# Kernel optimization log

Measured on AMD Instinct MI355X. Metric: run time of the kernel, lower is better.

The kernel has to match this reference:

```python
import jax, jax.numpy as jnp
import numpy as np

MEM_LEN = 1024
EPS = 1e-5


def _layer_norm(x, g, b):
    mu = jnp.mean(x, axis=-1, keepdims=True)
    var = jnp.mean((x - mu) ** 2, axis=-1, keepdims=True)
    return (x - mu) * jax.lax.rsqrt(var + EPS) * g + b


def _rel_shift(t):
    # t: [B, H, T, L] -> TXL pad->view->slice->view shift
    B, H, T, L = t.shape
    padded = jnp.concatenate([jnp.zeros((B, H, T, 1), t.dtype), t], axis=-1)
    padded = padded.reshape(B, H, L + 1, T)
    return padded[:, :, 1:, :].reshape(B, H, T, L)


def _pos_emb(length, d_model, dtype):
    inv_freq = 1.0 / (10000.0 ** (np.arange(0, d_model, 2, dtype=np.float32) / d_model))
    pos_seq = np.arange(length - 1, -1, -1, dtype=np.float32)
    sin_inp = np.outer(pos_seq, inv_freq)
    pe = np.concatenate([np.sin(sin_inp), np.cos(sin_inp)], axis=-1)
    return jnp.asarray(pe, dtype=dtype)


def setup_inputs() -> dict:
    key = jax.random.key(0)
    ks = jax.random.split(key, 12)
    B, T, M, D, H, Dff = 4, 1024, 1024, 1024, 16, 4096
    dh = D // H
    s = 1.0 / np.sqrt(D)
    return {
        "x": jax.random.normal(ks[0], (B, T, D), jnp.float32),
        "mem": jax.random.normal(ks[1], (B, M, D), jnp.float32),
        "Wq": jax.random.normal(ks[2], (D, D), jnp.float32) * s,
        "Wk": jax.random.normal(ks[3], (D, D), jnp.float32) * s,
        "Wv": jax.random.normal(ks[4], (D, D), jnp.float32) * s,
        "Wr": jax.random.normal(ks[5], (D, D), jnp.float32) * s,
        "Wo": jax.random.normal(ks[6], (D, D), jnp.float32) * s,
        "bias_u": jax.random.normal(ks[7], (H, dh), jnp.float32) * 0.02,
        "bias_v": jax.random.normal(ks[8], (H, dh), jnp.float32) * 0.02,
        "ln1_g": jnp.ones((D,), jnp.float32),
        "ln1_b": jnp.zeros((D,), jnp.float32),
        "ln2_g": jnp.ones((D,), jnp.float32),
        "ln2_b": jnp.zeros((D,), jnp.float32),
        "W1": jax.random.normal(ks[9], (D, Dff), jnp.float32) * s,
        "b1": jnp.zeros((Dff,), jnp.float32),
        "W2": jax.random.normal(ks[10], (Dff, D), jnp.float32) * (1.0 / np.sqrt(Dff)),
        "b2": jnp.zeros((D,), jnp.float32),
    }


def reference(x, mem, Wq, Wk, Wv, Wr, Wo, bias_u, bias_v,
              ln1_g, ln1_b, ln2_g, ln2_b, W1, b1, W2, b2):
    B, T, D = x.shape
    M = mem.shape[1]
    H, dh = bias_u.shape
    L = T + M
    scale = 1.0 / np.sqrt(dh)

    residual = x
    xn = _layer_norm(x, ln1_g, ln1_b)

    cat = jnp.concatenate([mem_n := mem, xn], axis=1) if False else jnp.concatenate([mem, xn], axis=1)
    # NOTE: torch concatenates raw memory states (not re-normalized) with norm_x.
    k = (cat @ Wk).reshape(B, L, H, dh).transpose(0, 2, 1, 3)      # [B,H,L,dh]
    v = (cat @ Wv).reshape(B, L, H, dh).transpose(0, 2, 1, 3)      # [B,H,L,dh]
    q = (xn @ Wq).reshape(B, T, H, dh).transpose(0, 2, 1, 3)       # [B,H,T,dh]

    pe = _pos_emb(L, D, x.dtype)                                   # [L,D]
    r = (pe @ Wr).reshape(L, H, dh).transpose(1, 0, 2)             # [H,L,dh]

    content = jnp.einsum("bhid,bhjd->bhij", q + bias_u[None, :, None, :], k)
    rel = jnp.einsum("bhid,hjd->bhij", q + bias_v[None, :, None, :], r)
    rel = _rel_shift(rel)

    attn = jax.nn.softmax((content + rel) * scale, axis=-1)        # [B,H,T,L]
    out = jnp.einsum("bhij,bhjd->bhid", attn, v)                   # [B,H,T,dh]
    out = out.transpose(0, 2, 1, 3).reshape(B, T, D) @ Wo

    x2 = residual + out
    xf = _layer_norm(x2, ln2_g, ln2_b)
    ff = jax.nn.gelu(xf @ W1 + b1, approximate=False) @ W2 + b2
    y = x2 + ff

    new_mem = jax.lax.stop_gradient(
        jnp.concatenate([mem, residual], axis=1)[:, -MEM_LEN:])
    return y, new_mem
```

## Files before the change

kernel.cpp:

```cpp
#include <hip/hip_runtime.h>
#include <hip/hip_bf16.h>

typedef short bf16x8 __attribute__((ext_vector_type(8)));
typedef float f32x4 __attribute__((ext_vector_type(4)));
typedef unsigned short u16;

__device__ __forceinline__ float bf2f(u16 u) {
    union { unsigned int i; float f; } x; x.i = ((unsigned int)u) << 16; return x.f;
}
__device__ __forceinline__ u16 f2bf(float f) {
    union { float f; unsigned int i; } x; x.f = f;
    unsigned int r = x.i + 0x7fff + ((x.i >> 16) & 1);
    return (u16)(r >> 16);
}
__device__ __forceinline__ f32x4 mfma16(bf16x8 a, bf16x8 b, f32x4 c) {
    return __builtin_amdgcn_mfma_f32_16x16x32_bf16(a, b, c, 0, 0, 0);
}
#define GLL16(lds_base, gsrc) \
    __builtin_amdgcn_global_load_lds((const __attribute__((address_space(1))) void*)(gsrc), \
                                     (__attribute__((address_space(3))) void*)(lds_base), 16, 0, 0)

__global__ __launch_bounds__(256)
void transpose_kernel(const float* __restrict__ in, u16* __restrict__ out, int R, int C) {
    __shared__ float t[32][33];
    const int c0 = blockIdx.x * 32, r0 = blockIdx.y * 32;
    const int tx = threadIdx.x & 31, ty = threadIdx.x >> 5;
#pragma unroll
    for (int i = 0; i < 32; i += 8) t[ty + i][tx] = in[(size_t)(r0 + ty + i) * C + c0 + tx];
    __syncthreads();
#pragma unroll
    for (int i = 0; i < 32; i += 8) out[(size_t)(c0 + ty + i) * R + r0 + tx] = f2bf(t[tx][ty + i]);
}

__global__ __launch_bounds__(256)
void convert_kernel(const float* __restrict__ in, u16* __restrict__ out) {
    const size_t i = ((size_t)blockIdx.x * 256 + threadIdx.x) * 8;
    const float4 a = *(const float4*)(in + i);
    const float4 b = *(const float4*)(in + i + 4);
    bf16x8 o;
    o[0] = (short)f2bf(a.x); o[1] = (short)f2bf(a.y);
    o[2] = (short)f2bf(a.z); o[3] = (short)f2bf(a.w);
    o[4] = (short)f2bf(b.x); o[5] = (short)f2bf(b.y);
    o[6] = (short)f2bf(b.z); o[7] = (short)f2bf(b.w);
    *(bf16x8*)(out + i) = o;
}

__global__ __launch_bounds__(256)
void pe_kernel(u16* __restrict__ pe) {
    const int idx = blockIdx.x * 256 + threadIdx.x;
    const int p = idx >> 10, d = idx & 1023;
    const float pos = (float)(2047 - p);
    const int k = d & 511;
    const float invf = powf(10000.f, ((float)(2 * k)) * (-1.f / 1024.f));
    const float a = pos * invf;
    pe[idx] = f2bf((d < 512) ? sinf(a) : cosf(a));
}

__global__ __launch_bounds__(256)
void ln_kernel(const float* __restrict__ inp, const float* __restrict__ gg,
               const float* __restrict__ bb, u16* __restrict__ outp) {
    const int row = blockIdx.x * 4 + (threadIdx.x >> 6);
    const int l = threadIdx.x & 63;
    const size_t base = (size_t)row * 1024 + l * 16;
    float v[16];
    const float4* p4 = (const float4*)(inp + base);
#pragma unroll
    for (int j = 0; j < 4; ++j) {
        float4 f = p4[j];
        v[j*4+0] = f.x; v[j*4+1] = f.y; v[j*4+2] = f.z; v[j*4+3] = f.w;
    }
    float s = 0.f, s2 = 0.f;
#pragma unroll
    for (int j = 0; j < 16; ++j) { s += v[j]; s2 += v[j] * v[j]; }
#pragma unroll
    for (int off = 1; off < 64; off <<= 1) {
        s += __shfl_xor(s, off, 64);
        s2 += __shfl_xor(s2, off, 64);
    }
    const float mu = s * 0.0009765625f;
    const float var = s2 * 0.0009765625f - mu * mu;
    const float rs = rsqrtf(var + 1e-5f);
#pragma unroll
    for (int j = 0; j < 16; ++j)
        outp[base + j] = f2bf((v[j] - mu) * rs * gg[l * 16 + j] + bb[l * 16 + j]);
}

template<int EPI, bool CATA>
__global__ __launch_bounds__(256)
void gemm_kernel(const u16* __restrict__ A, const u16* __restrict__ A2,
                 const u16* __restrict__ Wt, void* __restrict__ outp,
                 u16* __restrict__ out2, const float* __restrict__ cb1,
                 const float* __restrict__ cb2, const float* __restrict__ residp,
                 int Mdim, int Ndim, int Kdim) {
    __shared__ __attribute__((aligned(16))) u16 As[128 * 32];
    __shared__ __attribute__((aligned(16))) u16 Bs[128 * 32];
    const int tid = threadIdx.x;
    const int w = tid >> 6, l = tid & 63;
    const int wr = w >> 1, wc = w & 1;
    const int m0 = blockIdx.x * 128, n0 = blockIdx.y * 128;
    f32x4 acc[4][4] = {};

    for (int k0 = 0; k0 < Kdim; k0 += 32) {
        __syncthreads();
#pragma unroll
        for (int p = 0; p < 2; ++p) {
            const int ebase = (p * 4 + w) * 512;
            const int e = ebase + l * 8;
            const int row = e >> 5, colk = e & 31;
            const u16* srcA;
            if (CATA) {
                const int rr = m0 + row;
                const int bb_ = rr >> 11, pos = rr & 2047;
                srcA = (pos < 1024 ? A + ((size_t)(bb_ * 1024 + pos)) * 1024
                                   : A2 + ((size_t)(bb_ * 1024 + pos - 1024)) * 1024)
                       + (k0 + colk);
            } else {
                srcA = A + (size_t)(m0 + row) * Kdim + (k0 + colk);
            }
            const u16* srcB = Wt + (size_t)(n0 + row) * Kdim + (k0 + colk);
            GLL16(&As[ebase], srcA);
            GLL16(&Bs[ebase], srcB);
        }
        __syncthreads();
        bf16x8 af[4], bfr[4];
#pragma unroll
        for (int mi = 0; mi < 4; ++mi)
            af[mi] = *(const bf16x8*)&As[(wr * 64 + mi * 16 + (l & 15)) * 32 + (l >> 4) * 8];
#pragma unroll
        for (int ni = 0; ni < 4; ++ni)
            bfr[ni] = *(const bf16x8*)&Bs[(wc * 64 + ni * 16 + (l & 15)) * 32 + (l >> 4) * 8];
#pragma unroll
        for (int mi = 0; mi < 4; ++mi)
#pragma unroll
            for (int ni = 0; ni < 4; ++ni)
                acc[mi][ni] = mfma16(af[mi], bfr[ni], acc[mi][ni]);
    }

#pragma unroll
    for (int mi = 0; mi < 4; ++mi)
#pragma unroll
        for (int ni = 0; ni < 4; ++ni)
#pragma unroll
            for (int rg = 0; rg < 4; ++rg) {
                const int row = m0 + wr * 64 + mi * 16 + (l >> 4) * 4 + rg;
                const int col = n0 + wc * 64 + ni * 16 + (l & 15);
                const size_t idx = (size_t)row * Ndim + col;
                const float v = acc[mi][ni][rg];
                if (EPI == 0) {
                    ((u16*)outp)[idx] = f2bf(v);
                } else if (EPI == 1) {
                    ((u16*)outp)[idx] = f2bf(v + cb1[col]);
                    out2[idx] = f2bf(v + cb2[col]);
                } else if (EPI == 2) {
                    ((float*)outp)[idx] = v + residp[idx];
                } else if (EPI == 3) {
                    const float t = v + cb1[col];
                    ((u16*)outp)[idx] = f2bf(0.5f * t * (1.f + erff(t * 0.70710678118654752f)));
                } else {
                    ((float*)outp)[idx] = v + cb1[col] + residp[idx];
                }
            }
}

__global__ __launch_bounds__(256, 2)
void attn_kernel(const u16* __restrict__ qu, const u16* __restrict__ qv,
                 const u16* __restrict__ kcat, const u16* __restrict__ vcat,
                 const u16* __restrict__ rbuf, u16* __restrict__ outp) {
    constexpr int T = 1024, L = 2048, MM = 1024;
    __shared__ __attribute__((aligned(16))) u16 KtL[64 * 64];
    __shared__ __attribute__((aligned(16))) u16 RmL[128 * 64];
    __shared__ __attribute__((aligned(16))) u16 RwL[128 * 64];
    __shared__ __attribute__((aligned(16))) u16 Vt[64][72];
    __shared__ __attribute__((aligned(16))) u16 Pl[4][16][72];
    const int bid = blockIdx.x;
    const int g = (bid & 7) + 8 * (bid >> 7);
    const int it = (bid >> 3) & 15;
    const int h = g & 15, b = g >> 4;
    const int i0 = it * 64;
    const int tid = threadIdx.x;
    const int w = tid >> 6, l = tid & 63;
    const int lg = l >> 4, ll = l & 15;
    const int iw0 = i0 + w * 16;
    const int l8 = l >> 3;
    const int ssrc = ((l & 7) * 8) ^ (l8 << 3);
    const int sA = (lg * 8) ^ ((ll & 7) << 3);
    const int sB = (lg * 8 + 32) ^ ((ll & 7) << 3);

    bf16x8 quf[2], qvf[2];
    const int qc = h * 64 + lg * 8;
    {
        const size_t qrow = (size_t)(b * T + iw0 + ll);
        quf[0] = *(const bf16x8*)&qu[qrow * 1024 + qc];
        quf[1] = *(const bf16x8*)&qu[qrow * 1024 + qc + 32];
        qvf[0] = *(const bf16x8*)&qv[qrow * 1024 + qc];
        qvf[1] = *(const bf16x8*)&qv[qrow * 1024 + qc + 32];
    }
    const int r2 = iw0 + ll + 1;
    const size_t qrow2 = (size_t)(b * T + (r2 < T ? r2 : T - 1));
    const u16* kb = kcat + (size_t)b * L * 1024 + h * 64;
    const u16* vb = vcat + (size_t)b * L * 1024 + h * 64;
    const u16* rb = rbuf + h * 64;

    f32x4 o_acc[4] = {};
    float m_run[4] = {-1e30f, -1e30f, -1e30f, -1e30f};
    float l_run[4] = {0.f, 0.f, 0.f, 0.f};
    const int vjq = tid & 15, vdg = tid >> 4;

    for (int jt = 0; jt < 32; ++jt) {
        const int j0 = jt * 64;
        const bool main_blk = (j0 <= MM + i0 + 63);
        const bool wrap_blk = (j0 + 63 >= MM + i0 + 2);
        __syncthreads();
#pragma unroll
        for (int p = 0; p < 2; ++p) {
            const int k8 = w * 2 + p;
            GLL16(&KtL[k8 * 512], kb + (size_t)(j0 + k8 * 8 + l8) * 1024 + ssrc);
        }
        if (main_blk) {
            const long bm = (long)j0 + T - i0 - 64;
#pragma unroll
            for (int p = 0; p < 4; ++p) {
                const int k8 = w * 4 + p;
                GLL16(&RmL[k8 * 512], rb + (long)(bm + k8 * 8 + l8) * 1024 + ssrc);
            }
        }
        if (wrap_blk) {
            const long bw_ = (long)j0 - MM - i0 - 65;
#pragma unroll
            for (int p = 0; p < 4; ++p) {
                const int k8 = w * 4 + p;
                GLL16(&RwL[k8 * 512], rb + (long)(bw_ + k8 * 8 + l8) * 1024 + ssrc);
            }
        }
        {
            const u16* srcv = vb + (size_t)(j0 + vjq * 4) * 1024 + vdg * 4;
            const ushort4 r0 = *(const ushort4*)(srcv);
            const ushort4 r1 = *(const ushort4*)(srcv + 1024);
            const ushort4 r2w = *(const ushort4*)(srcv + 2048);
            const ushort4 r3 = *(const ushort4*)(srcv + 3072);
            const ushort4 c0 = {r0.x, r1.x, r2w.x, r3.x};
            const ushort4 c1 = {r0.y, r1.y, r2w.y, r3.y};
            const ushort4 c2 = {r0.z, r1.z, r2w.z, r3.z};
            const ushort4 c3 = {r0.w, r1.w, r2w.w, r3.w};
            *(ushort4*)&Vt[vdg * 4 + 0][vjq * 4] = c0;
            *(ushort4*)&Vt[vdg * 4 + 1][vjq * 4] = c1;
            *(ushort4*)&Vt[vdg * 4 + 2][vjq * 4] = c2;
            *(ushort4*)&Vt[vdg * 4 + 3][vjq * 4] = c3;
        }
        __syncthreads();

        f32x4 sv[4];
        __builtin_amdgcn_s_setprio(1);
#pragma unroll
        for (int ns = 0; ns < 4; ++ns) {
            const int rowb = (ns * 16 + ll) * 64;
            f32x4 a = {0.f, 0.f, 0.f, 0.f};
            a = mfma16(quf[0], *(const bf16x8*)&KtL[rowb + sA], a);
            a = mfma16(quf[1], *(const bf16x8*)&KtL[rowb + sB], a);
            sv[ns] = a;
        }
        __builtin_amdgcn_s_setprio(0);

        if (j0 <= MM + iw0 + 15) {
            const int trb = 48 - 16 * w;
            f32x4 gb[5];
#pragma unroll
            for (int cs = 0; cs < 5; ++cs) {
                const int rowb = (trb + cs * 16 + ll) * 64;
                f32x4 a = {0.f, 0.f, 0.f, 0.f};
                a = mfma16(qvf[0], *(const bf16x8*)&RmL[rowb + sA], a);
                a = mfma16(qvf[1], *(const bf16x8*)&RmL[rowb + sB], a);
                gb[cs] = a;
            }
#pragma unroll
            for (int r = 0; r < 4; ++r) {
                const int i_loc = lg * 4 + r;
                const int ig = iw0 + i_loc;
#pragma unroll
                for (int ns = 0; ns < 4; ++ns) {
                    const int j_loc = ns * 16 + ll;
                    const int c = j_loc + 15 - i_loc;
                    const int srcl = (l & 48) | (c & 15);
                    const float t0 = __shfl(gb[ns][r], srcl, 64);
                    const float t1 = __shfl(gb[ns + 1][r], srcl, 64);
                    const float gm = ((c >> 4) == ns) ? t0 : t1;
                    if (j0 + j_loc <= MM + ig) sv[ns][r] += gm;
                }
            }
        }
        if (j0 + 63 >= MM + iw0 + 2) {
            const bf16x8 qv2f0 = *(const bf16x8*)&qv[qrow2 * 1024 + qc];
            const bf16x8 qv2f1 = *(const bf16x8*)&qv[qrow2 * 1024 + qc + 32];
            const int trb = 48 - 16 * w;
            f32x4 gb[5];
#pragma unroll
            for (int cs = 0; cs < 5; ++cs) {
                const int rowb = (trb + cs * 16 + ll) * 64;
                f32x4 a = {0.f, 0.f, 0.f, 0.f};
                a = mfma16(qv2f0, *(const bf16x8*)&RwL[rowb + sA], a);
                a = mfma16(qv2f1, *(const bf16x8*)&RwL[rowb + sB], a);
                gb[cs] = a;
            }
#pragma unroll
            for (int r = 0; r < 4; ++r) {
                const int i_loc = lg * 4 + r;
                const int ig = iw0 + i_loc;
#pragma unroll
                for (int ns = 0; ns < 4; ++ns) {
                    const int j_loc = ns * 16 + ll;
                    const int c = j_loc + 15 - i_loc;
                    const int srcl = (l & 48) | (c & 15);
                    const float t0 = __shfl(gb[ns][r], srcl, 64);
                    const float t1 = __shfl(gb[ns + 1][r], srcl, 64);
                    const float gw = ((c >> 4) == ns) ? t0 : t1;
                    if (j0 + j_loc >= MM + ig + 2) sv[ns][r] += gw;
                }
            }
        }

#pragma unroll
        for (int r = 0; r < 4; ++r) {
            const int i_loc = lg * 4 + r;
            float s0 = sv[0][r] * 0.125f, s1 = sv[1][r] * 0.125f;
            float s2 = sv[2][r] * 0.125f, s3 = sv[3][r] * 0.125f;
            float pm = fmaxf(fmaxf(s0, s1), fmaxf(s2, s3));
            pm = fmaxf(pm, __shfl_xor(pm, 1, 64));
            pm = fmaxf(pm, __shfl_xor(pm, 2, 64));
            pm = fmaxf(pm, __shfl_xor(pm, 4, 64));
            pm = fmaxf(pm, __shfl_xor(pm, 8, 64));
            const float mnew = fmaxf(m_run[r], pm);
            const float alpha = __expf(m_run[r] - mnew);
            const float p0 = __expf(s0 - mnew), p1 = __expf(s1 - mnew);
            const float p2 = __expf(s2 - mnew), p3 = __expf(s3 - mnew);
            Pl[w][i_loc][0 * 16 + ll] = f2bf(p0);
            Pl[w][i_loc][1 * 16 + ll] = f2bf(p1);
            Pl[w][i_loc][2 * 16 + ll] = f2bf(p2);
            Pl[w][i_loc][3 * 16 + ll] = f2bf(p3);
            float ps = p0 + p1 + p2 + p3;
            ps += __shfl_xor(ps, 1, 64);
            ps += __shfl_xor(ps, 2, 64);
            ps += __shfl_xor(ps, 4, 64);
            ps += __shfl_xor(ps, 8, 64);
            l_run[r] = l_run[r] * alpha + ps;
            m_run[r] = mnew;
#pragma unroll
            for (int ns = 0; ns < 4; ++ns) o_acc[ns][r] *= alpha;
        }

        __builtin_amdgcn_s_setprio(1);
        const bf16x8 ap0 = *(const bf16x8*)&Pl[w][ll][lg * 8];
        const bf16x8 ap1 = *(const bf16x8*)&Pl[w][ll][32 + lg * 8];
#pragma unroll
        for (int ns = 0; ns < 4; ++ns) {
            const bf16x8 bv0 = *(const bf16x8*)&Vt[ns * 16 + ll][lg * 8];
            const bf16x8 bv1 = *(const bf16x8*)&Vt[ns * 16 + ll][32 + lg * 8];
            o_acc[ns] = mfma16(ap0, bv0, o_acc[ns]);
            o_acc[ns] = mfma16(ap1, bv1, o_acc[ns]);
        }
        __builtin_amdgcn_s_setprio(0);
    }

#pragma unroll
    for (int ns = 0; ns < 4; ++ns)
#pragma unroll
        for (int r = 0; r < 4; ++r) {
            const int row = iw0 + lg * 4 + r;
            outp[(size_t)(b * T + row) * 1024 + h * 64 + ns * 16 + ll] =
                f2bf(o_acc[ns][r] / l_run[r]);
        }
}

extern "C" void kernel_launch(void* const* d_in, const int* in_sizes, int n_in,
                              void* d_out, int out_size, void* d_ws, size_t ws_size,
                              hipStream_t stream) {
    const float* x    = (const float*)d_in[0];
    const float* mem  = (const float*)d_in[1];
    const float* Wq   = (const float*)d_in[2];
    const float* Wk   = (const float*)d_in[3];
    const float* Wv   = (const float*)d_in[4];
    const float* Wr   = (const float*)d_in[5];
    const float* Wo   = (const float*)d_in[6];
    const float* bu   = (const float*)d_in[7];
    const float* bv   = (const float*)d_in[8];
    const float* ln1g = (const float*)d_in[9];
    const float* ln1b = (const float*)d_in[10];
    const float* ln2g = (const float*)d_in[11];
    const float* ln2b = (const float*)d_in[12];
    const float* W1   = (const float*)d_in[13];
    const float* b1   = (const float*)d_in[14];
    const float* W2   = (const float*)d_in[15];
    const float* b2   = (const float*)d_in[16];

    float* y_out   = (float*)d_out;
    float* mem_out = (float*)d_out + 4194304;

    char* dob = (char*)d_out;
    u16* attno     = (u16*)(dob + 0);
    u16* pe        = (u16*)(dob + (size_t)8  * 1048576);
    u16* rbuf_base = (u16*)(dob + (size_t)12 * 1048576);
    u16* rbuf      = rbuf_base + 80 * 1024;
    char* dw = dob + (size_t)16 * 1048576 + 524288;
    u16* WqT = (u16*)(dw);
    u16* WkT = (u16*)(dw + (size_t)2 * 1048576);
    u16* WvT = (u16*)(dw + (size_t)4 * 1048576);
    u16* WrT = (u16*)(dw + (size_t)6 * 1048576);
    u16* WoT = (u16*)(dw + (size_t)8 * 1048576);

    char* ws = (char*)d_ws;
    const size_t MB = 1u << 20;
    u16*  xn    = (u16*)(ws + 0 * MB);
    u16*  x2n   = (u16*)(ws + 0 * MB);
    u16*  W2T   = (u16*)(ws + 0 * MB);
    u16*  qu    = (u16*)(ws + 8 * MB);
    float* x2f  = (float*)(ws + 8 * MB);
    u16*  qv    = (u16*)(ws + 16 * MB);
    u16*  kcat  = (u16*)(ws + 24 * MB);
    u16*  ffh   = (u16*)(ws + 24 * MB);
    u16*  vcat  = (u16*)(ws + 40 * MB);
    u16*  memb  = (u16*)(ws + 56 * MB);
    u16*  W1T   = (u16*)(ws + 56 * MB);

    transpose_kernel<<<dim3(32, 32), 256, 0, stream>>>(Wq, WqT, 1024, 1024);
    transpose_kernel<<<dim3(32, 32), 256, 0, stream>>>(Wk, WkT, 1024, 1024);
    transpose_kernel<<<dim3(32, 32), 256, 0, stream>>>(Wv, WvT, 1024, 1024);
    transpose_kernel<<<dim3(32, 32), 256, 0, stream>>>(Wr, WrT, 1024, 1024);
    transpose_kernel<<<dim3(32, 32), 256, 0, stream>>>(Wo, WoT, 1024, 1024);
    pe_kernel<<<8192, 256, 0, stream>>>(pe);
    convert_kernel<<<2048, 256, 0, stream>>>(mem, memb);
    ln_kernel<<<1024, 256, 0, stream>>>(x, ln1g, ln1b, xn);
    gemm_kernel<0, false><<<dim3(16, 8), 256, 0, stream>>>(pe, nullptr, WrT, rbuf, nullptr, nullptr, nullptr, nullptr, 2048, 1024, 1024);
    gemm_kernel<1, false><<<dim3(32, 8), 256, 0, stream>>>(xn, nullptr, WqT, qu, qv, bu, bv, nullptr, 4096, 1024, 1024);
    gemm_kernel<0, true><<<dim3(64, 8), 256, 0, stream>>>(memb, xn, WkT, kcat, nullptr, nullptr, nullptr, nullptr, 8192, 1024, 1024);
    gemm_kernel<0, true><<<dim3(64, 8), 256, 0, stream>>>(memb, xn, WvT, vcat, nullptr, nullptr, nullptr, nullptr, 8192, 1024, 1024);
    attn_kernel<<<1024, 256, 0, stream>>>(qu, qv, kcat, vcat, rbuf, attno);
    gemm_kernel<2, false><<<dim3(32, 8), 256, 0, stream>>>(attno, nullptr, WoT, x2f, nullptr, nullptr, nullptr, x, 4096, 1024, 1024);
    transpose_kernel<<<dim3(128, 32), 256, 0, stream>>>(W1, W1T, 1024, 4096);
    hipMemcpyAsync(mem_out, x, (size_t)4194304 * 4, hipMemcpyDeviceToDevice, stream);
    ln_kernel<<<1024, 256, 0, stream>>>(x2f, ln2g, ln2b, x2n);
    gemm_kernel<3, false><<<dim3(32, 32), 256, 0, stream>>>(x2n, nullptr, W1T, ffh, nullptr, b1, nullptr, nullptr, 4096, 4096, 1024);
    transpose_kernel<<<dim3(32, 128), 256, 0, stream>>>(W2, W2T, 4096, 1024);
    gemm_kernel<4, false><<<dim3(32, 8), 256, 0, stream>>>(ffh, nullptr, W2T, y_out, nullptr, b2, nullptr, x2f, 4096, 1024, 4096);
    (void)in_sizes; (void)n_in; (void)out_size; (void)ws_size;
}
```

Baseline: 599.8 us.

## Process 128 query rows per attention block so K/V/R tiles are reused twice

Each attention workgroup now covers 128 query rows instead of 64, with every wave handling two 16-row groups, so each K, V and positional tile loaded into LDS feeds twice as many rows. The grid is halved to 512 blocks and the launch bound drops to one block per SIMD-set, allowing more registers. The relative-position gather is also restructured to shuffle five sources once per row and select per column, instead of shuffling twice per column. In exchange, the larger LDS and register footprint lowers occupancy and gives fewer blocks to spread across the CUs. The rbuf padding offset is adjusted to match the larger R window.

```diff
diff --git a/kernel.cpp b/kernel.cpp
--- a/kernel.cpp
+++ b/kernel.cpp
@@ -162,53 +162,54 @@
             }
 }
 
-__global__ __launch_bounds__(256, 2)
+__global__ __launch_bounds__(256, 1)
 void attn_kernel(const u16* __restrict__ qu, const u16* __restrict__ qv,
                  const u16* __restrict__ kcat, const u16* __restrict__ vcat,
                  const u16* __restrict__ rbuf, u16* __restrict__ outp) {
     constexpr int T = 1024, L = 2048, MM = 1024;
     __shared__ __attribute__((aligned(16))) u16 KtL[64 * 64];
-    __shared__ __attribute__((aligned(16))) u16 RmL[128 * 64];
-    __shared__ __attribute__((aligned(16))) u16 RwL[128 * 64];
+    __shared__ __attribute__((aligned(16))) u16 RmL[192 * 64];
+    __shared__ __attribute__((aligned(16))) u16 RwL[192 * 64];
     __shared__ __attribute__((aligned(16))) u16 Vt[64][72];
-    __shared__ __attribute__((aligned(16))) u16 Pl[4][16][72];
+    __shared__ __attribute__((aligned(16))) u16 Pl[4][32][72];
     const int bid = blockIdx.x;
-    const int g = (bid & 7) + 8 * (bid >> 7);
-    const int it = (bid >> 3) & 15;
+    const int it = bid >> 6;
+    const int g = bid & 63;
     const int h = g & 15, b = g >> 4;
-    const int i0 = it * 64;
+    const int i0 = it * 128;
     const int tid = threadIdx.x;
     const int w = tid >> 6, l = tid & 63;
     const int lg = l >> 4, ll = l & 15;
-    const int iw0 = i0 + w * 16;
     const int l8 = l >> 3;
     const int ssrc = ((l & 7) * 8) ^ (l8 << 3);
     const int sA = (lg * 8) ^ ((ll & 7) << 3);
     const int sB = (lg * 8 + 32) ^ ((ll & 7) << 3);
-
-    bf16x8 quf[2], qvf[2];
     const int qc = h * 64 + lg * 8;
-    {
-        const size_t qrow = (size_t)(b * T + iw0 + ll);
-        quf[0] = *(const bf16x8*)&qu[qrow * 1024 + qc];
-        quf[1] = *(const bf16x8*)&qu[qrow * 1024 + qc + 32];
-        qvf[0] = *(const bf16x8*)&qv[qrow * 1024 + qc];
-        qvf[1] = *(const bf16x8*)&qv[qrow * 1024 + qc + 32];
+
+    bf16x8 quf[2][2], qvf[2][2];
+#pragma unroll
+    for (int rg = 0; rg < 2; ++rg) {
+        const size_t qrow = (size_t)(b * T + i0 + (w * 2 + rg) * 16 + ll);
+        quf[rg][0] = *(const bf16x8*)&qu[qrow * 1024 + qc];
+        quf[rg][1] = *(const bf16x8*)&qu[qrow * 1024 + qc + 32];
+        qvf[rg][0] = *(const bf16x8*)&qv[qrow * 1024 + qc];
+        qvf[rg][1] = *(const bf16x8*)&qv[qrow * 1024 + qc + 32];
     }
-    const int r2 = iw0 + ll + 1;
-    const size_t qrow2 = (size_t)(b * T + (r2 < T ? r2 : T - 1));
     const u16* kb = kcat + (size_t)b * L * 1024 + h * 64;
     const u16* vb = vcat + (size_t)b * L * 1024 + h * 64;
     const u16* rb = rbuf + h * 64;
 
-    f32x4 o_acc[4] = {};
-    float m_run[4] = {-1e30f, -1e30f, -1e30f, -1e30f};
-    float l_run[4] = {0.f, 0.f, 0.f, 0.f};
+    f32x4 o_acc[2][4] = {};
+    float m_run[2][4], l_run[2][4];
+#pragma unroll
+    for (int rg = 0; rg < 2; ++rg)
+#pragma unroll
+        for (int r = 0; r < 4; ++r) { m_run[rg][r] = -1e30f; l_run[rg][r] = 0.f; }
     const int vjq = tid & 15, vdg = tid >> 4;
 
     for (int jt = 0; jt < 32; ++jt) {
         const int j0 = jt * 64;
-        const bool main_blk = (j0 <= MM + i0 + 63);
+        const bool main_blk = (j0 <= MM + i0 + 127);
         const bool wrap_blk = (j0 + 63 >= MM + i0 + 2);
         __syncthreads();
 #pragma unroll
@@ -217,18 +218,18 @@
             GLL16(&KtL[k8 * 512], kb + (size_t)(j0 + k8 * 8 + l8) * 1024 + ssrc);
         }
         if (main_blk) {
-            const long bm = (long)j0 + T - i0 - 64;
-#pragma unroll
-            for (int p = 0; p < 4; ++p) {
-                const int k8 = w * 4 + p;
+            const long bm = (long)j0 + T - i0 - 128;
+#pragma unroll
+            for (int p = 0; p < 6; ++p) {
+                const int k8 = w * 6 + p;
                 GLL16(&RmL[k8 * 512], rb + (long)(bm + k8 * 8 + l8) * 1024 + ssrc);
             }
         }
         if (wrap_blk) {
-            const long bw_ = (long)j0 - MM - i0 - 65;
-#pragma unroll
-            for (int p = 0; p < 4; ++p) {
-                const int k8 = w * 4 + p;
+            const long bw_ = (long)j0 - MM - i0 - 129;
+#pragma unroll
+            for (int p = 0; p < 6; ++p) {
+                const int k8 = w * 6 + p;
                 GLL16(&RwL[k8 * 512], rb + (long)(bw_ + k8 * 8 + l8) * 1024 + ssrc);
             }
         }
@@ -249,125 +250,157 @@
         }
         __syncthreads();
 
-        f32x4 sv[4];
+        f32x4 sv[2][4];
         __builtin_amdgcn_s_setprio(1);
 #pragma unroll
         for (int ns = 0; ns < 4; ++ns) {
             const int rowb = (ns * 16 + ll) * 64;
-            f32x4 a = {0.f, 0.f, 0.f, 0.f};
-            a = mfma16(quf[0], *(const bf16x8*)&KtL[rowb + sA], a);
-            a = mfma16(quf[1], *(const bf16x8*)&KtL[rowb + sB], a);
-            sv[ns] = a;
+            const bf16x8 k0 = *(const bf16x8*)&KtL[rowb + sA];
+            const bf16x8 k1 = *(const bf16x8*)&KtL[rowb + sB];
+#pragma unroll
+            for (int rg = 0; rg < 2; ++rg) {
+                f32x4 a = {0.f, 0.f, 0.f, 0.f};
+                a = mfma16(quf[rg][0], k0, a);
+                a = mfma16(quf[rg][1], k1, a);
+                sv[rg][ns] = a;
+            }
         }
         __builtin_amdgcn_s_setprio(0);
 
-        if (j0 <= MM + iw0 + 15) {
-            const int trb = 48 - 16 * w;
-            f32x4 gb[5];
-#pragma unroll
-            for (int cs = 0; cs < 5; ++cs) {
-                const int rowb = (trb + cs * 16 + ll) * 64;
-                f32x4 a = {0.f, 0.f, 0.f, 0.f};
-                a = mfma16(qvf[0], *(const bf16x8*)&RmL[rowb + sA], a);
-                a = mfma16(qvf[1], *(const bf16x8*)&RmL[rowb + sB], a);
-                gb[cs] = a;
-            }
+#pragma unroll
+        for (int rg = 0; rg < 2; ++rg) {
+            const int q = w * 2 + rg;
+            const int iw0q = i0 + q * 16;
+            const int trb = 112 - 16 * q;
+            if (j0 <= MM + iw0q + 15) {
+                f32x4 gb[5];
+#pragma unroll
+                for (int cs = 0; cs < 5; ++cs) {
+                    const int rowb = (trb + cs * 16 + ll) * 64;
+                    f32x4 a = {0.f, 0.f, 0.f, 0.f};
+                    a = mfma16(qvf[rg][0], *(const bf16x8*)&RmL[rowb + sA], a);
+                    a = mfma16(qvf[rg][1], *(const bf16x8*)&RmL[rowb + sB], a);
+                    gb[cs] = a;
+                }
+#pragma unroll
+                for (int r = 0; r < 4; ++r) {
+                    const int i_loc = lg * 4 + r;
+                    const int srcl = (l & 48) | ((ll + 15 - i_loc) & 15);
+                    const float sh0 = __shfl(gb[0][r], srcl, 64);
+                    const float sh1 = __shfl(gb[1][r], srcl, 64);
+                    const float sh2 = __shfl(gb[2][r], srcl, 64);
+                    const float sh3 = __shfl(gb[3][r], srcl, 64);
+                    const float sh4 = __shfl(gb[4][r], srcl, 64);
+                    const bool hi = (ll > i_loc);
+                    const int thr = MM + iw0q + i_loc - j0;
+                    const float e0 = hi ? sh1 : sh0;
+                    const float e1 = hi ? sh2 : sh1;
+                    const float e2 = hi ? sh3 : sh2;
+                    const float e3 = hi ? sh4 : sh3;
+                    if (ll <= thr)      sv[rg][0][r] += e0;
+                    if (16 + ll <= thr) sv[rg][1][r] += e1;
+                    if (32 + ll <= thr) sv[rg][2][r] += e2;
+                    if (48 + ll <= thr) sv[rg][3][r] += e3;
+                }
+            }
+            if (j0 + 63 >= MM + iw0q + 2) {
+                const int r2v = iw0q + ll + 1;
+                const size_t qrow2 = (size_t)(b * T + (r2v < T ? r2v : T - 1));
+                const bf16x8 q20 = *(const bf16x8*)&qv[qrow2 * 1024 + qc];
+                const bf16x8 q21 = *(const bf16x8*)&qv[qrow2 * 1024 + qc + 32];
+                f32x4 gb[5];
+#pragma unroll
+                for (int cs = 0; cs < 5; ++cs) {
+                    const int rowb = (trb + cs * 16 + ll) * 64;
+                    f32x4 a = {0.f, 0.f, 0.f, 0.f};
+                    a = mfma16(q20, *(const bf16x8*)&RwL[rowb + sA], a);
+                    a = mfma16(q21, *(const bf16x8*)&RwL[rowb + sB], a);
+                    gb[cs] = a;
+                }
+#pragma unroll
+                for (int r = 0; r < 4; ++r) {
+                    const int i_loc = lg * 4 + r;
+                    const int srcl = (l & 48) | ((ll + 15 - i_loc) & 15);
+                    const float sh0 = __shfl(gb[0][r], srcl, 64);
+                    const float sh1 = __shfl(gb[1][r], srcl, 64);
+                    const float sh2 = __shfl(gb[2][r], srcl, 64);
+                    const float sh3 = __shfl(gb[3][r], srcl, 64);
+                    const float sh4 = __shfl(gb[4][r], srcl, 64);
+                    const bool hi = (ll > i_loc);
+                    const int thr2 = MM + iw0q + i_loc - j0 + 2;
+                    const float e0 = hi ? sh1 : sh0;
+                    const float e1 = hi ? sh2 : sh1;
+                    const float e2 = hi ? sh3 : sh2;
+                    const float e3 = hi ? sh4 : sh3;
+                    if (ll >= thr2)      sv[rg][0][r] += e0;
+                    if (16 + ll >= thr2) sv[rg][1][r] += e1;
+                    if (32 + ll >= thr2) sv[rg][2][r] += e2;
+                    if (48 + ll >= thr2) sv[rg][3][r] += e3;
+                }
+            }
+        }
+
+#pragma unroll
+        for (int rg = 0; rg < 2; ++rg)
 #pragma unroll
             for (int r = 0; r < 4; ++r) {
                 const int i_loc = lg * 4 + r;
-                const int ig = iw0 + i_loc;
-#pragma unroll
-                for (int ns = 0; ns < 4; ++ns) {
-                    const int j_loc = ns * 16 + ll;
-                    const int c = j_loc + 15 - i_loc;
-                    const int srcl = (l & 48) | (c & 15);
-                    const float t0 = __shfl(gb[ns][r], srcl, 64);
-                    const float t1 = __shfl(gb[ns + 1][r], srcl, 64);
-                    const float gm = ((c >> 4) == ns) ? t0 : t1;
-                    if (j0 + j_loc <= MM + ig) sv[ns][r] += gm;
-                }
-            }
-        }
-        if (j0 + 63 >= MM + iw0 + 2) {
-            const bf16x8 qv2f0 = *(const bf16x8*)&qv[qrow2 * 1024 + qc];
-            const bf16x8 qv2f1 = *(const bf16x8*)&qv[qrow2 * 1024 + qc + 32];
-            const int trb = 48 - 16 * w;
-            f32x4 gb[5];
-#pragma unroll
-            for (int cs = 0; cs < 5; ++cs) {
-                const int rowb = (trb + cs * 16 + ll) * 64;
-                f32x4 a = {0.f, 0.f, 0.f, 0.f};
-                a = mfma16(qv2f0, *(const bf16x8*)&RwL[rowb + sA], a);
-                a = mfma16(qv2f1, *(const bf16x8*)&RwL[rowb + sB], a);
-                gb[cs] = a;
-            }
-#pragma unroll
-            for (int r = 0; r < 4; ++r) {
-                const int i_loc = lg * 4 + r;
-                const int ig = iw0 + i_loc;
-#pragma unroll
-                for (int ns = 0; ns < 4; ++ns) {
-                    const int j_loc = ns * 16 + ll;
-                    const int c = j_loc + 15 - i_loc;
-                    const int srcl = (l & 48) | (c & 15);
-                    const float t0 = __shfl(gb[ns][r], srcl, 64);
-                    const float t1 = __shfl(gb[ns + 1][r], srcl, 64);
-                    const float gw = ((c >> 4) == ns) ? t0 : t1;
-                    if (j0 + j_loc >= MM + ig + 2) sv[ns][r] += gw;
-                }
-            }
-        }
-
-#pragma unroll
-        for (int r = 0; r < 4; ++r) {
-            const int i_loc = lg * 4 + r;
-            float s0 = sv[0][r] * 0.125f, s1 = sv[1][r] * 0.125f;
-            float s2 = sv[2][r] * 0.125f, s3 = sv[3][r] * 0.125f;
-            float pm = fmaxf(fmaxf(s0, s1), fmaxf(s2, s3));
-            pm = fmaxf(pm, __shfl_xor(pm, 1, 64));
-            pm = fmaxf(pm, __shfl_xor(pm, 2, 64));
-            pm = fmaxf(pm, __shfl_xor(pm, 4, 64));
-            pm = fmaxf(pm, __shfl_xor(pm, 8, 64));
-            const float mnew = fmaxf(m_run[r], pm);
-            const float alpha = __expf(m_run[r] - mnew);
-            const float p0 = __expf(s0 - mnew), p1 = __expf(s1 - mnew);
-            const float p2 = __expf(s2 - mnew), p3 = __expf(s3 - mnew);
-            Pl[w][i_loc][0 * 16 + ll] = f2bf(p0);
-            Pl[w][i_loc][1 * 16 + ll] = f2bf(p1);
-            Pl[w][i_loc][2 * 16 + ll] = f2bf(p2);
-            Pl[w][i_loc][3 * 16 + ll] = f2bf(p3);
-            float ps = p0 + p1 + p2 + p3;
-            ps += __shfl_xor(ps, 1, 64);
-            ps += __shfl_xor(ps, 2, 64);
-            ps += __shfl_xor(ps, 4, 64);
-            ps += __shfl_xor(ps, 8, 64);
-            l_run[r] = l_run[r] * alpha + ps;
-            m_run[r] = mnew;
-#pragma unroll
-            for (int ns = 0; ns < 4; ++ns) o_acc[ns][r] *= alpha;
-        }
+                const float s0 = sv[rg][0][r] * 0.125f, s1 = sv[rg][1][r] * 0.125f;
+                const float s2 = sv[rg][2][r] * 0.125f, s3 = sv[rg][3][r] * 0.125f;
+                float pm = fmaxf(fmaxf(s0, s1), fmaxf(s2, s3));
+                pm = fmaxf(pm, __shfl_xor(pm, 1, 64));
+                pm = fmaxf(pm, __shfl_xor(pm, 2, 64));
+                pm = fmaxf(pm, __shfl_xor(pm, 4, 64));
+                pm = fmaxf(pm, __shfl_xor(pm, 8, 64));
+                const float mnew = fmaxf(m_run[rg][r], pm);
+                const float alpha = __expf(m_run[rg][r] - mnew);
+                const float p0 = __expf(s0 - mnew), p1 = __expf(s1 - mnew);
+                const float p2 = __expf(s2 - mnew), p3 = __expf(s3 - mnew);
+                Pl[w][rg * 16 + i_loc][0 * 16 + ll] = f2bf(p0);
+                Pl[w][rg * 16 + i_loc][1 * 16 + ll] = f2bf(p1);
+                Pl[w][rg * 16 + i_loc][2 * 16 + ll] = f2bf(p2);
+                Pl[w][rg * 16 + i_loc][3 * 16 + ll] = f2bf(p3);
+                float ps = p0 + p1 + p2 + p3;
+                ps += __shfl_xor(ps, 1, 64);
+                ps += __shfl_xor(ps, 2, 64);
+                ps += __shfl_xor(ps, 4, 64);
+                ps += __shfl_xor(ps, 8, 64);
+                l_run[rg][r] = l_run[rg][r] * alpha + ps;
+                m_run[rg][r] = mnew;
+#pragma unroll
+                for (int ns = 0; ns < 4; ++ns) o_acc[rg][ns][r] *= alpha;
+            }
 
         __builtin_amdgcn_s_setprio(1);
-        const bf16x8 ap0 = *(const bf16x8*)&Pl[w][ll][lg * 8];
-        const bf16x8 ap1 = *(const bf16x8*)&Pl[w][ll][32 + lg * 8];
+        bf16x8 ap[2][2];
+#pragma unroll
+        for (int rg = 0; rg < 2; ++rg) {
+            ap[rg][0] = *(const bf16x8*)&Pl[w][rg * 16 + ll][lg * 8];
+            ap[rg][1] = *(const bf16x8*)&Pl[w][rg * 16 + ll][32 + lg * 8];
+        }
 #pragma unroll
         for (int ns = 0; ns < 4; ++ns) {
             const bf16x8 bv0 = *(const bf16x8*)&Vt[ns * 16 + ll][lg * 8];
             const bf16x8 bv1 = *(const bf16x8*)&Vt[ns * 16 + ll][32 + lg * 8];
-            o_acc[ns] = mfma16(ap0, bv0, o_acc[ns]);
-            o_acc[ns] = mfma16(ap1, bv1, o_acc[ns]);
+#pragma unroll
+            for (int rg = 0; rg < 2; ++rg) {
+                o_acc[rg][ns] = mfma16(ap[rg][0], bv0, o_acc[rg][ns]);
+                o_acc[rg][ns] = mfma16(ap[rg][1], bv1, o_acc[rg][ns]);
+            }
         }
         __builtin_amdgcn_s_setprio(0);
     }
 
 #pragma unroll
-    for (int ns = 0; ns < 4; ++ns)
-#pragma unroll
-        for (int r = 0; r < 4; ++r) {
-            const int row = iw0 + lg * 4 + r;
-            outp[(size_t)(b * T + row) * 1024 + h * 64 + ns * 16 + ll] =
-                f2bf(o_acc[ns][r] / l_run[r]);
-        }
+    for (int rg = 0; rg < 2; ++rg)
+#pragma unroll
+        for (int ns = 0; ns < 4; ++ns)
+#pragma unroll
+            for (int r = 0; r < 4; ++r) {
+                const int row = i0 + (w * 2 + rg) * 16 + lg * 4 + r;
+                outp[(size_t)(b * T + row) * 1024 + h * 64 + ns * 16 + ll] =
+                    f2bf(o_acc[rg][ns][r] / l_run[rg][r]);
+            }
 }
 
 extern "C" void kernel_launch(void* const* d_in, const int* in_sizes, int n_in,
@@ -398,8 +431,8 @@
     u16* attno     = (u16*)(dob + 0);
     u16* pe        = (u16*)(dob + (size_t)8  * 1048576);
     u16* rbuf_base = (u16*)(dob + (size_t)12 * 1048576);
-    u16* rbuf      = rbuf_base + 80 * 1024;
-    char* dw = dob + (size_t)16 * 1048576 + 524288;
+    u16* rbuf      = rbuf_base + 144 * 1024;
+    char* dw = dob + (size_t)17 * 1048576;
     u16* WqT = (u16*)(dw);
     u16* WkT = (u16*)(dw + (size_t)2 * 1048576);
     u16* WvT = (u16*)(dw + (size_t)4 * 1048576);
@@ -432,7 +465,7 @@
     gemm_kernel<1, false><<<dim3(32, 8), 256, 0, stream>>>(xn, nullptr, WqT, qu, qv, bu, bv, nullptr, 4096, 1024, 1024);
     gemm_kernel<0, true><<<dim3(64, 8), 256, 0, stream>>>(memb, xn, WkT, kcat, nullptr, nullptr, nullptr, nullptr, 8192, 1024, 1024);
     gemm_kernel<0, true><<<dim3(64, 8), 256, 0, stream>>>(memb, xn, WvT, vcat, nullptr, nullptr, nullptr, nullptr, 8192, 1024, 1024);
-    attn_kernel<<<1024, 256, 0, stream>>>(qu, qv, kcat, vcat, rbuf, attno);
+    attn_kernel<<<512, 256, 0, stream>>>(qu, qv, kcat, vcat, rbuf, attno);
     gemm_kernel<2, false><<<dim3(32, 8), 256, 0, stream>>>(attno, nullptr, WoT, x2f, nullptr, nullptr, nullptr, x, 4096, 1024, 1024);
     transpose_kernel<<<dim3(128, 32), 256, 0, stream>>>(W1, W1T, 1024, 4096);
     hipMemcpyAsync(mem_out, x, (size_t)4194304 * 4, hipMemcpyDeviceToDevice, stream);
```

New measurement: 694.0 us. 15.7% more time.

## Fuse K and V projection GEMMs and streamline rel-shift shuffle logic

Applied to the files above, without the earlier changes.

Replaces the two separate K and V projection GEMMs with one kernel that loads each A tile once and multiplies it against both WkT and WvT, keeping two accumulator sets. This halves the activation reads and removes one kernel launch. The cost is twice the accumulator registers, which may lower occupancy or cause spills. Separately, the relative-position shift in attention now shuffles the five gb fragments once per row and selects with a single boolean, instead of doing two shuffles per column slice.

```diff
diff --git a/kernel.cpp b/kernel.cpp
--- a/kernel.cpp
+++ b/kernel.cpp
@@ -159,6 +159,70 @@
                 } else {
                     ((float*)outp)[idx] = v + cb1[col] + residp[idx];
                 }
+            }
+}
+
+__global__ __launch_bounds__(256)
+void gemm_kv_kernel(const u16* __restrict__ A, const u16* __restrict__ A2,
+                    const u16* __restrict__ WtK, const u16* __restrict__ WtV,
+                    u16* __restrict__ outK, u16* __restrict__ outV) {
+    __shared__ __attribute__((aligned(16))) u16 As[128 * 32];
+    __shared__ __attribute__((aligned(16))) u16 Bk[128 * 32];
+    __shared__ __attribute__((aligned(16))) u16 Bv[128 * 32];
+    const int tid = threadIdx.x;
+    const int w = tid >> 6, l = tid & 63;
+    const int wr = w >> 1, wc = w & 1;
+    const int m0 = blockIdx.x * 128, n0 = blockIdx.y * 128;
+    f32x4 acck[4][4] = {};
+    f32x4 accv[4][4] = {};
+
+    for (int k0 = 0; k0 < 1024; k0 += 32) {
+        __syncthreads();
+#pragma unroll
+        for (int p = 0; p < 2; ++p) {
+            const int ebase = (p * 4 + w) * 512;
+            const int e = ebase + l * 8;
+            const int row = e >> 5, colk = e & 31;
+            const int rr = m0 + row;
+            const int bb_ = rr >> 11, pos = rr & 2047;
+            const u16* srcA = (pos < 1024 ? A + ((size_t)(bb_ * 1024 + pos)) * 1024
+                                          : A2 + ((size_t)(bb_ * 1024 + pos - 1024)) * 1024)
+                              + (k0 + colk);
+            GLL16(&As[ebase], srcA);
+            GLL16(&Bk[ebase], WtK + (size_t)(n0 + row) * 1024 + (k0 + colk));
+            GLL16(&Bv[ebase], WtV + (size_t)(n0 + row) * 1024 + (k0 + colk));
+        }
+        __syncthreads();
+        bf16x8 af[4], bkf[4], bvf[4];
+#pragma unroll
+        for (int mi = 0; mi < 4; ++mi)
+            af[mi] = *(const bf16x8*)&As[(wr * 64 + mi * 16 + (l & 15)) * 32 + (l >> 4) * 8];
+#pragma unroll
+        for (int ni = 0; ni < 4; ++ni) {
+            const int off = (wc * 64 + ni * 16 + (l & 15)) * 32 + (l >> 4) * 8;
+            bkf[ni] = *(const bf16x8*)&Bk[off];
+            bvf[ni] = *(const bf16x8*)&Bv[off];
+        }
+#pragma unroll
+        for (int mi = 0; mi < 4; ++mi)
+#pragma unroll
+            for (int ni = 0; ni < 4; ++ni) {
+                acck[mi][ni] = mfma16(af[mi], bkf[ni], acck[mi][ni]);
+                accv[mi][ni] = mfma16(af[mi], bvf[ni], accv[mi][ni]);
+            }
+    }
+
+#pragma unroll
+    for (int mi = 0; mi < 4; ++mi)
+#pragma unroll
+        for (int ni = 0; ni < 4; ++ni)
+#pragma unroll
+            for (int rg = 0; rg < 4; ++rg) {
+                const int row = m0 + wr * 64 + mi * 16 + (l >> 4) * 4 + rg;
+                const int col = n0 + wc * 64 + ni * 16 + (l & 15);
+                const size_t idx = (size_t)row * 1024 + col;
+                outK[idx] = f2bf(acck[mi][ni][rg]);
+                outV[idx] = f2bf(accv[mi][ni][rg]);
             }
 }
 
@@ -275,17 +339,22 @@
 #pragma unroll
             for (int r = 0; r < 4; ++r) {
                 const int i_loc = lg * 4 + r;
-                const int ig = iw0 + i_loc;
-#pragma unroll
-                for (int ns = 0; ns < 4; ++ns) {
-                    const int j_loc = ns * 16 + ll;
-                    const int c = j_loc + 15 - i_loc;
-                    const int srcl = (l & 48) | (c & 15);
-                    const float t0 = __shfl(gb[ns][r], srcl, 64);
-                    const float t1 = __shfl(gb[ns + 1][r], srcl, 64);
-                    const float gm = ((c >> 4) == ns) ? t0 : t1;
-                    if (j0 + j_loc <= MM + ig) sv[ns][r] += gm;
-                }
+                const int srcl = (l & 48) | ((ll + 15 - i_loc) & 15);
+                const float sh0 = __shfl(gb[0][r], srcl, 64);
+                const float sh1 = __shfl(gb[1][r], srcl, 64);
+                const float sh2 = __shfl(gb[2][r], srcl, 64);
+                const float sh3 = __shfl(gb[3][r], srcl, 64);
+                const float sh4 = __shfl(gb[4][r], srcl, 64);
+                const bool hi = (ll > i_loc);
+                const int thr = MM + iw0 + i_loc - j0;
+                const float e0 = hi ? sh1 : sh0;
+                const float e1 = hi ? sh2 : sh1;
+                const float e2 = hi ? sh3 : sh2;
+                const float e3 = hi ? sh4 : sh3;
+                if (ll <= thr)      sv[0][r] += e0;
+                if (16 + ll <= thr) sv[1][r] += e1;
+                if (32 + ll <= thr) sv[2][r] += e2;
+                if (48 + ll <= thr) sv[3][r] += e3;
             }
         }
         if (j0 + 63 >= MM + iw0 + 2) {
@@ -304,25 +373,30 @@
 #pragma unroll
             for (int r = 0; r < 4; ++r) {
                 const int i_loc = lg * 4 + r;
-                const int ig = iw0 + i_loc;
-#pragma unroll
-                for (int ns = 0; ns < 4; ++ns) {
-                    const int j_loc = ns * 16 + ll;
-                    const int c = j_loc + 15 - i_loc;
-                    const int srcl = (l & 48) | (c & 15);
-                    const float t0 = __shfl(gb[ns][r], srcl, 64);
-                    const float t1 = __shfl(gb[ns + 1][r], srcl, 64);
-                    const float gw = ((c >> 4) == ns) ? t0 : t1;
-                    if (j0 + j_loc >= MM + ig + 2) sv[ns][r] += gw;
-                }
+                const int srcl = (l & 48) | ((ll + 15 - i_loc) & 15);
+                const float sh0 = __shfl(gb[0][r], srcl, 64);
+                const float sh1 = __shfl(gb[1][r], srcl, 64);
+                const float sh2 = __shfl(gb[2][r], srcl, 64);
+                const float sh3 = __shfl(gb[3][r], srcl, 64);
+                const float sh4 = __shfl(gb[4][r], srcl, 64);
+                const bool hi = (ll > i_loc);
+                const int thr2 = MM + iw0 + i_loc - j0 + 2;
+                const float e0 = hi ? sh1 : sh0;
+                const float e1 = hi ? sh2 : sh1;
+                const float e2 = hi ? sh3 : sh2;
+                const float e3 = hi ? sh4 : sh3;
+                if (ll >= thr2)      sv[0][r] += e0;
+                if (16 + ll >= thr2) sv[1][r] += e1;
+                if (32 + ll >= thr2) sv[2][r] += e2;
+                if (48 + ll >= thr2) sv[3][r] += e3;
             }
         }
 
 #pragma unroll
         for (int r = 0; r < 4; ++r) {
             const int i_loc = lg * 4 + r;
-            float s0 = sv[0][r] * 0.125f, s1 = sv[1][r] * 0.125f;
-            float s2 = sv[2][r] * 0.125f, s3 = sv[3][r] * 0.125f;
+            const float s0 = sv[0][r] * 0.125f, s1 = sv[1][r] * 0.125f;
+            const float s2 = sv[2][r] * 0.125f, s3 = sv[3][r] * 0.125f;
             float pm = fmaxf(fmaxf(s0, s1), fmaxf(s2, s3));
             pm = fmaxf(pm, __shfl_xor(pm, 1, 64));
             pm = fmaxf(pm, __shfl_xor(pm, 2, 64));
@@ -430,8 +504,7 @@
     ln_kernel<<<1024, 256, 0, stream>>>(x, ln1g, ln1b, xn);
     gemm_kernel<0, false><<<dim3(16, 8), 256, 0, stream>>>(pe, nullptr, WrT, rbuf, nullptr, nullptr, nullptr, nullptr, 2048, 1024, 1024);
     gemm_kernel<1, false><<<dim3(32, 8), 256, 0, stream>>>(xn, nullptr, WqT, qu, qv, bu, bv, nullptr, 4096, 1024, 1024);
-    gemm_kernel<0, true><<<dim3(64, 8), 256, 0, stream>>>(memb, xn, WkT, kcat, nullptr, nullptr, nullptr, nullptr, 8192, 1024, 1024);
-    gemm_kernel<0, true><<<dim3(64, 8), 256, 0, stream>>>(memb, xn, WvT, vcat, nullptr, nullptr, nullptr, nullptr, 8192, 1024, 1024);
+    gemm_kv_kernel<<<dim3(64, 8), 256, 0, stream>>>(memb, xn, WkT, WvT, kcat, vcat);
     attn_kernel<<<1024, 256, 0, stream>>>(qu, qv, kcat, vcat, rbuf, attno);
     gemm_kernel<2, false><<<dim3(32, 8), 256, 0, stream>>>(attno, nullptr, WoT, x2f, nullptr, nullptr, nullptr, x, 4096, 1024, 1024);
     transpose_kernel<<<dim3(128, 32), 256, 0, stream>>>(W1, W1T, 1024, 4096);
```

Measured after the change: 594.9 us. Within noise of the previous version (-0.8%).
